# Kernel optimization log

Hardware: AMD Instinct MI355X
Metric: run time of the kernel (lower is better)

## Reference

```python
import math
import jax, jax.numpy as jnp
import numpy as np

V, D, H, L, FH = 32000, 384, 6, 6, 1536
B, S = 38, 256
HD = D // H


def setup_inputs() -> dict:
    key = jax.random.key(0)
    ks = jax.random.split(key, 16)
    sc = 0.02
    inp = {
        "x": jax.random.randint(ks[0], (B, S), 1, V, dtype=jnp.int32),
        "targets": jax.random.randint(ks[1], (B, S), 0, V, dtype=jnp.int32),
        "emb": jax.random.normal(ks[2], (V, D), jnp.float32) * sc,
        "Wqkv": jax.random.normal(ks[3], (L, 3 * D, D), jnp.float32) * sc,
        "bqkv": jnp.zeros((L, 3 * D), jnp.float32),
        "Wo": jax.random.normal(ks[4], (L, D, D), jnp.float32) * sc,
        "bo": jnp.zeros((L, D), jnp.float32),
        "gamma1": jnp.ones((L, D), jnp.float32),
        "beta1": jnp.zeros((L, D), jnp.float32),
        "W1": jax.random.normal(ks[5], (L, FH, D), jnp.float32) * sc,
        "b1": jnp.zeros((L, FH), jnp.float32),
        "W2": jax.random.normal(ks[6], (L, D, FH), jnp.float32) * sc,
        "b2": jnp.zeros((L, D), jnp.float32),
        "gamma2": jnp.ones((L, D), jnp.float32),
        "beta2": jnp.zeros((L, D), jnp.float32),
        "Wout": jax.random.normal(ks[7], (V, D), jnp.float32) * sc,
        "bout": jnp.zeros((V,), jnp.float32),
    }
    return inp


def _pos_encoding(seq_len, d_model):
    even_i = jnp.arange(0, d_model, 2, dtype=jnp.float32)
    denom = jnp.power(10000.0, even_i / d_model)  # (D/2,)
    pos = jnp.arange(seq_len, dtype=jnp.float32)[:, None]  # (S,1)
    even_pe = jnp.sin(pos / denom)
    odd_pe = jnp.cos(pos / denom)
    return jnp.stack([even_pe, odd_pe], axis=2).reshape(seq_len, d_model)


def _layer_norm(x, gamma, beta, eps=1e-5):
    mean = x.mean(axis=-1, keepdims=True)
    var = ((x - mean) ** 2).mean(axis=-1, keepdims=True)
    return gamma * (x - mean) / jnp.sqrt(var + eps) + beta


def _build_mask(x_ids, seq_len):
    # replicate the data-dependent pad mask: take the row with most non-pad
    # tokens, count its leading non-zeros -> max_length
    pad = (x_ids != 0)
    idx = jnp.argmax(pad.sum(axis=1))
    row = x_ids[idx]
    has_zero = jnp.any(row == 0)
    max_len = jnp.where(has_zero, jnp.argmax(row == 0), seq_len)
    i = jnp.arange(seq_len)[:, None]
    j = jnp.arange(seq_len)[None, :]
    allowed = (j <= i) & ~((i >= max_len) & (j >= max_len))
    return jnp.where(allowed, 0.0, -jnp.inf).astype(jnp.float32)  # (S,S)


def _forward(x, targets, emb, Wqkv, bqkv, Wo, bo, gamma1, beta1, W1, b1,
             W2, b2, gamma2, beta2, Wout, bout):
    Bn, Sn = x.shape
    h = emb[x] * math.sqrt(D) + _pos_encoding(Sn, D)[None]  # (B,S,D)
    mask = _build_mask(x, Sn)
    inv_sqrt_dk = 1.0 / math.sqrt(HD)

    def layer(h, p):
        (Wq, bq, Wo_, bo_, g1, be1, W1_, b1_, W2_, b2_, g2, be2) = p
        qkv = h @ Wq.T + bq  # (B,S,3D)
        qkv = qkv.reshape(Bn, Sn, H, 3 * HD).transpose(0, 2, 1, 3)  # (B,H,S,3hd)
        q, k, v = jnp.split(qkv, 3, axis=-1)
        scores = jnp.einsum('bhqd,bhkd->bhqk', q, k) * inv_sqrt_dk + mask
        attn = jax.nn.softmax(scores, axis=-1)
        vals = jnp.einsum('bhqk,bhkd->bhqd', attn, v)
        vals = vals.transpose(0, 2, 1, 3).reshape(Bn, Sn, D)
        att_out = vals @ Wo_.T + bo_
        h = _layer_norm(h + att_out, g1, be1)
        ffn = jax.nn.gelu(h @ W1_.T + b1_, approximate=False) @ W2_.T + b2_
        h = _layer_norm(h + ffn, g2, be2)
        return h, None

    params = (Wqkv, bqkv, Wo, bo, gamma1, beta1, W1, b1, W2, b2, gamma2, beta2)
    h, _ = jax.lax.scan(layer, h, params)

    logits = h @ Wout.T + bout  # (B,S,V)
    logp = jax.nn.log_softmax(logits, axis=-1)
    nll = -jnp.take_along_axis(logp, targets[..., None].astype(jnp.int32), axis=-1)[..., 0]
    loss = nll.mean()
    return logits, loss


def reference(x, targets, emb, Wqkv, bqkv, Wo, bo, gamma1, beta1, W1, b1,
              W2, b2, gamma2, beta2, Wout, bout):
    return _forward(x, targets, emb, Wqkv, bqkv, Wo, bo, gamma1, beta1,
                    W1, b1, W2, b2, gamma2, beta2, Wout, bout)
```

## Files before the change

### kernel.cpp

```cpp
#include <hip/hip_runtime.h>
#include <hip/hip_bf16.h>
#include <math.h>

#define VSZ 32000
#define DSZ 384
#define HSZ 6
#define LSZ 6
#define FHSZ 1536
#define BSZ 38
#define SSZ 256
#define HDSZ 64
#define NROW (BSZ*SSZ)
#define D3 (3*DSZ)
#define NTB256 (VSZ/256)

typedef __bf16 bf16;
typedef __attribute__((ext_vector_type(8))) __bf16 bf16x8;
typedef __attribute__((ext_vector_type(4))) __bf16 bf16x4;
typedef __attribute__((ext_vector_type(4))) float f32x4;

__device__ __forceinline__ void gload16(const bf16* g, bf16* l) {
  __builtin_amdgcn_global_load_lds((const __attribute__((address_space(1))) void*)g,
                                   (__attribute__((address_space(3))) void*)l, 16, 0, 0);
}

__device__ __forceinline__ int xcd_swz(int orig, int nwg) {
  int q = nwg >> 3, r = nwg & 7;
  int xcd = orig & 7, lin = orig >> 3;
  return (xcd < r ? xcd*(q+1) : r*(q+1) + (xcd - r)*q) + lin;
}

__device__ __forceinline__ float fast_erf(float x) {
  float ax = fabsf(x);
  float t = 1.0f / fmaf(0.3275911f, ax, 1.0f);
  float p = fmaf(t, 1.061405429f, -1.453152027f);
  p = fmaf(p, t, 1.421413741f);
  p = fmaf(p, t, -0.284496736f);
  p = fmaf(p, t, 0.254829592f);
  float y = 1.0f - p*t*__expf(-ax*ax);
  return copysignf(y, x);
}

struct CvtDesc { const float* s0; bf16* d0; const float* s1; bf16* d1;
                 const float* s2; bf16* d2; const float* s3; bf16* d3;
                 const float* s4; bf16* d4; };
#define C0 663552
#define C1 884736
#define C2 1769472
#define C3 2654208
#define C4 5726208
__global__ __launch_bounds__(256) void cvt_all(CvtDesc dd) {
  int i = blockIdx.x*256 + threadIdx.x;
  int st = gridDim.x*256;
  for (; i < C4; i += st) {
    const float* s; bf16* d; int o;
    if      (i < C0) { s = dd.s0; d = dd.d0; o = i; }
    else if (i < C1) { s = dd.s1; d = dd.d1; o = i - C0; }
    else if (i < C2) { s = dd.s2; d = dd.d2; o = i - C1; }
    else if (i < C3) { s = dd.s3; d = dd.d3; o = i - C2; }
    else             { s = dd.s4; d = dd.d4; o = i - C3; }
    f32x4 v = __builtin_nontemporal_load((const f32x4*)s + o);
    bf16x4 ov = { (bf16)v[0], (bf16)v[1], (bf16)v[2], (bf16)v[3] };
    *(bf16x4*)(d + 4*(size_t)o) = ov;
  }
}

__global__ __launch_bounds__(256) void pe_k(float* __restrict__ pe) {
  const float c = 2.0f/384.0f*13.287712379549449f;
  int i = blockIdx.x*256 + threadIdx.x;
  int s = i / DSZ, d = i - s*DSZ;
  int ii = d >> 1;
  float ang = (float)s * exp2f(-(float)ii * c);
  pe[i] = (d & 1) ? cosf(ang) : sinf(ang);
}

__global__ __launch_bounds__(256) void embed_k(const int* __restrict__ x,
    const float* __restrict__ emb, const float* __restrict__ pe,
    float* __restrict__ h, bf16* __restrict__ hb) {
  const float scale = 19.595917942265423f;
  int i4 = blockIdx.x*256 + threadIdx.x;
  int st = gridDim.x*256;
  for (; i4 < NROW*(DSZ/4); i4 += st) {
    int r = i4 / (DSZ/4), c4 = (i4 - r*(DSZ/4))*4;
    int tok = x[r];
    int s = r & (SSZ-1);
    f32x4 e = *((const f32x4*)(emb + (size_t)tok*DSZ + c4));
    f32x4 p = *((const f32x4*)(pe + (size_t)s*DSZ + c4));
    f32x4 v = { e[0]*scale + p[0], e[1]*scale + p[1],
                e[2]*scale + p[2], e[3]*scale + p[3] };
    *(f32x4*)(h + (size_t)i4*4) = v;
    bf16x4 o = { (bf16)v[0], (bf16)v[1], (bf16)v[2], (bf16)v[3] };
    *(bf16x4*)(hb + (size_t)i4*4) = o;
  }
}

template<int MODE>
__global__ __launch_bounds__(256) void gemm_bt(const bf16* __restrict__ A,
    const bf16* __restrict__ Bm, const float* __restrict__ bias,
    bf16* __restrict__ Cv, int N, int K) {
  __shared__ __align__(16) bf16 As[2][128*64];
  __shared__ __align__(16) bf16 Bs[2][128*64];
  const int tid = threadIdx.x;
  const int lane = tid & 63, wid = tid >> 6;

  const int GX = gridDim.x, GY = gridDim.y;
  int orig = blockIdx.y*GX + blockIdx.x;
  int swz = xcd_swz(orig, GX*GY);
  int by = swz / GX, bx = swz - (swz/GX)*GX;

  const int wm = (wid >> 1) * 64, wn = (wid & 1) * 64;
  const int lr = lane & 15, lk = (lane >> 4) * 8;
  const int sx = (lr & 7) * 8;

  f32x4 acc[4][4];
  f32x4 zz = {0.f, 0.f, 0.f, 0.f};
#pragma unroll
  for (int m = 0; m < 4; ++m)
#pragma unroll
    for (int n = 0; n < 4; ++n) acc[m][n] = zz;

  const bf16* Ab = A + (size_t)by*128*K;
  const bf16* Bb = Bm + (size_t)bx*128*K;
  const int nk = K >> 6;

  auto STAGE = [&](int buf, int kt) {
#pragma unroll
    for (int c = 0; c < 4; ++c) {
      int chunk = c*256 + tid;
      int row = chunk >> 3, sub = chunk & 7;
      int scol = (sub ^ (row & 7)) * 8;
      gload16(Ab + (size_t)row*K + kt*64 + scol, &As[buf][chunk*8]);
      gload16(Bb + (size_t)row*K + kt*64 + scol, &Bs[buf][chunk*8]);
    }
  };

  STAGE(0, 0);
  __syncthreads();
  int cur = 0;
  for (int kt = 0; kt < nk; ++kt) {
    if (kt + 1 < nk) STAGE(cur ^ 1, kt + 1);
#pragma unroll
    for (int kk = 0; kk < 2; ++kk) {
      bf16x8 af[4], bfr[4];
#pragma unroll
      for (int m = 0; m < 4; ++m)
        af[m] = *(const bf16x8*)(&As[cur][(wm + m*16 + lr)*64 + ((kk*32 + lk) ^ sx)]);
#pragma unroll
      for (int n = 0; n < 4; ++n)
        bfr[n] = *(const bf16x8*)(&Bs[cur][(wn + n*16 + lr)*64 + ((kk*32 + lk) ^ sx)]);
#pragma unroll
      for (int m = 0; m < 4; ++m)
#pragma unroll
        for (int n = 0; n < 4; ++n)
          acc[m][n] = __builtin_amdgcn_mfma_f32_16x16x32_bf16(af[m], bfr[n], acc[m][n], 0, 0, 0);
    }
    __syncthreads();
    cur ^= 1;
  }

  float bv[4];
#pragma unroll
  for (int n = 0; n < 4; ++n) bv[n] = bias[bx*128 + wn + n*16 + lr];
  const int r0 = (lane >> 4) * 4;
#pragma unroll
  for (int m = 0; m < 4; ++m) {
#pragma unroll
    for (int r = 0; r < 4; ++r) {
      size_t row = (size_t)by*128 + wm + m*16 + r0 + r;
#pragma unroll
      for (int n = 0; n < 4; ++n) {
        float v = acc[m][n][r] + bv[n];
        size_t ci = row*(size_t)N + (size_t)(bx*128 + wn + n*16 + lr);
        if (MODE == 1) Cv[ci] = (bf16)v;
        else {
          v = 0.5f*v*(1.0f + fast_erf(v*0.70710678118654752f));
          Cv[ci] = (bf16)v;
        }
      }
    }
  }
}

template<int NS>
__global__ __launch_bounds__(256) void gemm_sk(const bf16* __restrict__ A,
    const bf16* __restrict__ Bm, const float* __restrict__ bias,
    bf16* __restrict__ P, int N, int K) {
  __shared__ __align__(16) bf16 As[2][128*64];
  __shared__ __align__(16) bf16 Bs[2][128*64];
  const int tid = threadIdx.x;
  const int lane = tid & 63, wid = tid >> 6;
  const int slice = blockIdx.z;
  const int Ksl = K / NS, kb = slice * Ksl;

  const int GX = gridDim.x, GY = gridDim.y;
  int orig = blockIdx.y*GX + blockIdx.x;
  int swz = xcd_swz(orig, GX*GY);
  int by = swz / GX, bx = swz - (swz/GX)*GX;

  const int wm = (wid >> 1) * 64, wn = (wid & 1) * 64;
  const int lr = lane & 15, lk = (lane >> 4) * 8;
  const int sx = (lr & 7) * 8;

  f32x4 acc[4][4];
  f32x4 zz = {0.f, 0.f, 0.f, 0.f};
#pragma unroll
  for (int m = 0; m < 4; ++m)
#pragma unroll
    for (int n = 0; n < 4; ++n) acc[m][n] = zz;

  const bf16* Ab = A + (size_t)by*128*K + kb;
  const bf16* Bb = Bm + (size_t)bx*128*K + kb;
  const int nk = Ksl >> 6;

  auto STAGE = [&](int buf, int kt) {
#pragma unroll
    for (int c = 0; c < 4; ++c) {
      int chunk = c*256 + tid;
      int row = chunk >> 3, sub = chunk & 7;
      int scol = (sub ^ (row & 7)) * 8;
      gload16(Ab + (size_t)row*K + kt*64 + scol, &As[buf][chunk*8]);
      gload16(Bb + (size_t)row*K + kt*64 + scol, &Bs[buf][chunk*8]);
    }
  };

  STAGE(0, 0);
  __syncthreads();
  int cur = 0;
  for (int kt = 0; kt < nk; ++kt) {
    if (kt + 1 < nk) STAGE(cur ^ 1, kt + 1);
#pragma unroll
    for (int kk = 0; kk < 2; ++kk) {
      bf16x8 af[4], bfr[4];
#pragma unroll
      for (int m = 0; m < 4; ++m)
        af[m] = *(const bf16x8*)(&As[cur][(wm + m*16 + lr)*64 + ((kk*32 + lk) ^ sx)]);
#pragma unroll
      for (int n = 0; n < 4; ++n)
        bfr[n] = *(const bf16x8*)(&Bs[cur][(wn + n*16 + lr)*64 + ((kk*32 + lk) ^ sx)]);
#pragma unroll
      for (int m = 0; m < 4; ++m)
#pragma unroll
        for (int n = 0; n < 4; ++n)
          acc[m][n] = __builtin_amdgcn_mfma_f32_16x16x32_bf16(af[m], bfr[n], acc[m][n], 0, 0, 0);
    }
    __syncthreads();
    cur ^= 1;
  }

  float bv[4];
#pragma unroll
  for (int n = 0; n < 4; ++n)
    bv[n] = (slice == 0) ? bias[bx*128 + wn + n*16 + lr] : 0.0f;
  const int r0 = (lane >> 4) * 4;
  bf16* Pw = P + (size_t)slice*NROW*N;
#pragma unroll
  for (int m = 0; m < 4; ++m) {
#pragma unroll
    for (int r = 0; r < 4; ++r) {
      size_t row = (size_t)by*128 + wm + m*16 + r0 + r;
#pragma unroll
      for (int n = 0; n < 4; ++n) {
        size_t ci = row*(size_t)N + (size_t)(bx*128 + wn + n*16 + lr);
        Pw[ci] = (bf16)(acc[m][n][r] + bv[n]);
      }
    }
  }
}

__global__ __launch_bounds__(512, 2) void gemm256_lse(const bf16* __restrict__ A,
    const bf16* __restrict__ Bm, const float* __restrict__ bias,
    float* __restrict__ C, float* __restrict__ pmax, float* __restrict__ psum) {
  __shared__ __align__(16) bf16 As[4][256*32];
  __shared__ __align__(16) bf16 Bs[4][256*32];
  __shared__ float sm_m[4][256], sm_s[4][256];
  const int K = DSZ, N = VSZ;
  const int tid = threadIdx.x;
  const int lane = tid & 63, wid = tid >> 6;

  const int GX = gridDim.x, GY = gridDim.y;
  int orig = blockIdx.y*GX + blockIdx.x;
  int swz = xcd_swz(orig, GX*GY);
  int bx = swz / GY, by = swz - (swz/GY)*GY;

  const int wm = (wid >> 2) * 128, wn = (wid & 3) * 64;
  const int lr = lane & 15, lk = (lane >> 4) * 8;

  f32x4 acc[8][4];
  f32x4 zz = {0.f, 0.f, 0.f, 0.f};
#pragma unroll
  for (int m = 0; m < 8; ++m)
#pragma unroll
    for (int n = 0; n < 4; ++n) acc[m][n] = zz;

  const bf16* Ab = A + (size_t)by*256*K;
  const bf16* Bb = Bm + (size_t)bx*256*K;
  const int nk = 12;

  auto STAGE = [&](int buf, int kt) {
#pragma unroll
    for (int c = 0; c < 2; ++c) {
      int chunk = c*512 + tid;
      int row = chunk >> 2, sub = chunk & 3;
      int scol = (sub ^ ((row >> 1) & 3)) * 8;
      gload16(Ab + (size_t)row*K + kt*32 + scol, &As[buf][chunk*8]);
      gload16(Bb + (size_t)row*K + kt*32 + scol, &Bs[buf][chunk*8]);
    }
  };

  STAGE(0, 0); STAGE(1, 1); STAGE(2, 2);
  for (int kt = 0; kt < nk; ++kt) {
    if (kt < nk - 2)      asm volatile("s_waitcnt vmcnt(8)" ::: "memory");
    else if (kt == nk-2)  asm volatile("s_waitcnt vmcnt(4)" ::: "memory");
    else                  asm volatile("s_waitcnt vmcnt(0)" ::: "memory");
    __builtin_amdgcn_s_barrier();
    __builtin_amdgcn_sched_barrier(0);
    const int buf = kt & 3;
    bf16x8 af[8], bfr[4];
#pragma unroll
    for (int n = 0; n < 4; ++n) {
      int row = wn + n*16 + lr;
      bfr[n] = *(const bf16x8*)(&Bs[buf][row*32 + (lk ^ (((row >> 1) & 3)*8))]);
    }
#pragma unroll
    for (int m = 0; m < 8; ++m) {
      int row = wm + m*16 + lr;
      af[m] = *(const bf16x8*)(&As[buf][row*32 + (lk ^ (((row >> 1) & 3)*8))]);
    }
#pragma unroll
    for (int m = 0; m < 8; ++m)
#pragma unroll
      for (int n = 0; n < 4; ++n)
        acc[m][n] = __builtin_amdgcn_mfma_f32_16x16x32_bf16(af[m], bfr[n], acc[m][n], 0, 0, 0);
    if (kt + 3 < nk) STAGE((kt + 3) & 3, kt + 3);
    __builtin_amdgcn_s_barrier();
  }

  float bv[4];
#pragma unroll
  for (int n = 0; n < 4; ++n) bv[n] = bias[bx*256 + wn + n*16 + lr];
  const int r0 = (lane >> 4) * 4;

#pragma unroll
  for (int m = 0; m < 8; ++m) {
#pragma unroll
    for (int r = 0; r < 4; ++r) {
      const int rl = wm + m*16 + r0 + r;
      size_t row = (size_t)by*256 + rl;
      float v0 = acc[m][0][r] + bv[0], v1 = acc[m][1][r] + bv[1];
      float v2 = acc[m][2][r] + bv[2], v3 = acc[m][3][r] + bv[3];
      size_t cb = row*(size_t)N + (size_t)(bx*256 + wn + lr);
      __builtin_nontemporal_store(v0, &C[cb]);
      __builtin_nontemporal_store(v1, &C[cb + 16]);
      __builtin_nontemporal_store(v2, &C[cb + 32]);
      __builtin_nontemporal_store(v3, &C[cb + 48]);
      float mx = fmaxf(fmaxf(v0, v1), fmaxf(v2, v3));
#pragma unroll
      for (int o = 1; o <= 8; o <<= 1) mx = fmaxf(mx, __shfl_xor(mx, o));
      float s = __expf(v0-mx) + __expf(v1-mx) + __expf(v2-mx) + __expf(v3-mx);
#pragma unroll
      for (int o = 1; o <= 8; o <<= 1) s += __shfl_xor(s, o);
      if (lr == 0) { sm_m[wid & 3][rl] = mx; sm_s[wid & 3][rl] = s; }
    }
  }
  __syncthreads();
  if (tid < 256) {
    float m = -1e30f, s = 0.f;
#pragma unroll
    for (int c = 0; c < 4; ++c) {
      float mi = sm_m[c][tid], si = sm_s[c][tid];
      float nm = fmaxf(m, mi);
      s = s*__expf(m - nm) + si*__expf(mi - nm);
      m = nm;
    }
    size_t row = (size_t)by*256 + tid;
    pmax[row*NTB256 + bx] = m;
    psum[row*NTB256 + bx] = s;
  }
}

__global__ __launch_bounds__(256) void attn_mfma(const bf16* __restrict__ qkv,
                                                 bf16* __restrict__ vals) {
  __shared__ __align__(16) ushort Ks[256*72];
  __shared__ __align__(16) ushort Vt[64*264];
  const int tid = threadIdx.x;
  const int lane = tid & 63, w = tid >> 6;
  const int lo = lane & 15, hi = lane >> 4;
  const int bid = blockIdx.x;
  const int qt = bid & 3, bh = bid >> 2;
  const int b = bh / HSZ, hh = bh - b*HSZ;
  const int nkr = (qt + 1) * 64;
  const int qb = qt*64 + w*16;
  const int ntile = qt*4 + w + 1;
  const int kkmax = (ntile + 1) >> 1;

  {
    const int jr = tid >> 3, cc = (tid & 7) * 8;
    for (int p = 0; p < (qt+1)*2; ++p) {
      int j = p*32 + jr;
      const bf16* base = qkv + ((size_t)(b*SSZ + j))*D3 + hh*192 + 64 + cc;
      uint4 kq = *(const uint4*)base;
      *(uint2*)(&Ks[j*72 + cc])     = make_uint2(kq.x, kq.y);
      *(uint2*)(&Ks[j*72 + cc + 4]) = make_uint2(kq.z, kq.w);
    }
  }
  for (int k = tid; k < nkr; k += 256) {
    const bf16* vrow = qkv + ((size_t)(b*SSZ + k))*D3 + hh*192 + 128;
#pragma unroll
    for (int c = 0; c < 8; ++c) {
      uint4 vv = *(const uint4*)(vrow + c*8);
      const ushort* u = (const ushort*)&vv;
#pragma unroll
      for (int j = 0; j < 8; ++j)
        Vt[(c*8 + j)*264 + k] = u[j];
    }
  }

  bf16x8 qf0, qf1;
  {
    const bf16* qrow = qkv + ((size_t)(b*SSZ + qb + lo))*D3 + hh*192 + hi*8;
    qf0 = *(const bf16x8*)(qrow);
    qf1 = *(const bf16x8*)(qrow + 32);
  }
  __syncthreads();

  f32x4 zz = {0.f, 0.f, 0.f, 0.f};
  f32x4 sacc[16];
#pragma unroll
  for (int n = 0; n < 16; ++n) sacc[n] = zz;
#pragma unroll
  for (int n = 0; n < 16; ++n)
    if (n < ntile) {
      const bf16* kb0 = (const bf16*)&Ks[(n*16 + lo)*72 + hi*8];
      bf16x8 bf0 = *(const bf16x8*)(kb0);
      bf16x8 bf1 = *(const bf16x8*)(kb0 + 32);
      sacc[n] = __builtin_amdgcn_mfma_f32_16x16x32_bf16(qf0, bf0, sacc[n], 0, 0, 0);
      sacc[n] = __builtin_amdgcn_mfma_f32_16x16x32_bf16(qf1, bf1, sacc[n], 0, 0, 0);
    }
  __syncthreads();

  float mrow[4] = {-1e30f, -1e30f, -1e30f, -1e30f};
#pragma unroll
  for (int n = 0; n < 16; ++n)
    if (n < ntile) {
#pragma unroll
      for (int r = 0; r < 4; ++r) {
        int kcol = n*16 + lo, qi = qb + hi*4 + r;
        float s = (kcol <= qi) ? sacc[n][r]*0.125f : -1e30f;
        sacc[n][r] = s;
        mrow[r] = fmaxf(mrow[r], s);
      }
    }
#pragma unroll
  for (int r = 0; r < 4; ++r)
#pragma unroll
    for (int o = 1; o <= 8; o <<= 1)
      mrow[r] = fmaxf(mrow[r], __shfl_xor(mrow[r], o));

  ushort* Pl = &Ks[w*64*72];
  float lsum[4] = {0.f, 0.f, 0.f, 0.f};
#pragma unroll
  for (int n = 0; n < 16; ++n)
    if (n < 2*kkmax) {
#pragma unroll
      for (int r = 0; r < 4; ++r) {
        float e = 0.f;
        if (n < ntile) { e = __expf(sacc[n][r] - mrow[r]); lsum[r] += e; }
        bf16 eb = (bf16)e;
        Pl[(hi*4 + r)*264 + n*16 + lo] = *(const ushort*)&eb;
      }
    }
#pragma unroll
  for (int r = 0; r < 4; ++r)
#pragma unroll
    for (int o = 1; o <= 8; o <<= 1)
      lsum[r] += __shfl_xor(lsum[r], o);

  asm volatile("s_waitcnt lgkmcnt(0)" ::: "memory");

  f32x4 oacc[4];
#pragma unroll
  for (int nd = 0; nd < 4; ++nd) oacc[nd] = zz;
#pragma unroll
  for (int kk = 0; kk < 8; ++kk)
    if (kk < kkmax) {
      bf16x8 pf = *(const bf16x8*)((const bf16*)&Pl[lo*264 + kk*32 + hi*8]);
#pragma unroll
      for (int nd = 0; nd < 4; ++nd) {
        bf16x8 vf = *(const bf16x8*)((const bf16*)&Vt[(nd*16 + lo)*264 + kk*32 + hi*8]);
        oacc[nd] = __builtin_amdgcn_mfma_f32_16x16x32_bf16(pf, vf, oacc[nd], 0, 0, 0);
      }
    }

#pragma unroll
  for (int r = 0; r < 4; ++r) {
    float inv = 1.0f / lsum[r];
    size_t row = (size_t)(b*SSZ + qb + hi*4 + r);
#pragma unroll
    for (int nd = 0; nd < 4; ++nd)
      vals[row*DSZ + hh*64 + nd*16 + lo] = (bf16)(oacc[nd][r] * inv);
  }
}

template<int NS>
__global__ __launch_bounds__(256) void ln_sum(const bf16* __restrict__ P,
    const float* __restrict__ gamma, const float* __restrict__ beta,
    float* __restrict__ h, bf16* __restrict__ hb) {
  const int t = threadIdx.x;
  const int lane = t & 63, w = t >> 6;
  const int row = blockIdx.x*4 + w;
  const size_t base = (size_t)row*DSZ;
  float v[6];
  float s = 0.f;
#pragma unroll
  for (int k = 0; k < 6; ++k) {
    int idx = lane + k*64;
    float acc = h[base + idx];
#pragma unroll
    for (int sl = 0; sl < NS; ++sl)
      acc += (float)P[(size_t)sl*NROW*DSZ + base + idx];
    v[k] = acc;
    s += acc;
  }
#pragma unroll
  for (int o = 32; o; o >>= 1) s += __shfl_xor(s, o);
  float mean = s * (1.0f/DSZ);
  float s2 = 0.f;
#pragma unroll
  for (int k = 0; k < 6; ++k) { float dv = v[k] - mean; s2 += dv*dv; }
#pragma unroll
  for (int o = 32; o; o >>= 1) s2 += __shfl_xor(s2, o);
  float rstd = rsqrtf(s2 * (1.0f/DSZ) + 1e-5f);
#pragma unroll
  for (int k = 0; k < 6; ++k) {
    int idx = lane + k*64;
    float outv = gamma[idx]*(v[k] - mean)*rstd + beta[idx];
    h[base + idx] = outv;
    hb[base + idx] = (bf16)outv;
  }
}

__global__ __launch_bounds__(256) void loss_merge(const float* __restrict__ pmax,
    const float* __restrict__ psum, const float* __restrict__ logits,
    const int* __restrict__ tg, float* __restrict__ nll, int ntb) {
  const int t = threadIdx.x;
  const int lane = t & 63, w = t >> 6;
  const int row = blockIdx.x*4 + w;
  float m = -1e30f, s = 0.f;
  for (int i = lane; i < ntb; i += 64) {
    float mi = pmax[(size_t)row*ntb + i], si = psum[(size_t)row*ntb + i];
    float nm = fmaxf(m, mi);
    s = s*__expf(m - nm) + si*__expf(mi - nm);
    m = nm;
  }
#pragma unroll
  for (int o = 32; o; o >>= 1) {
    float mo = __shfl_xor(m, o), so = __shfl_xor(s, o);
    float nm = fmaxf(m, mo);
    s = s*__expf(m - nm) + so*__expf(mo - nm);
    m = nm;
  }
  if (lane == 0)
    nll[row] = (m + logf(s)) - logits[(size_t)row*VSZ + tg[row]];
}

__global__ __launch_bounds__(256) void loss_final(const float* __restrict__ nll,
                                                  float* __restrict__ out) {
  __shared__ float red[4];
  const int t = threadIdx.x;
  const int lane = t & 63, w = t >> 6;
  float s = 0.f;
  for (int i = t; i < NROW; i += 256) s += nll[i];
#pragma unroll
  for (int o = 32; o; o >>= 1) s += __shfl_xor(s, o);
  if (lane == 0) red[w] = s;
  __syncthreads();
  if (t == 0) out[0] = (red[0]+red[1]+red[2]+red[3]) * (1.0f/NROW);
}

extern "C" void kernel_launch(void* const* d_in, const int* in_sizes, int n_in,
                              void* d_out, int out_size, void* d_ws, size_t ws_size,
                              hipStream_t stream) {
  (void)in_sizes; (void)n_in; (void)out_size; (void)ws_size;
  const int*   x       = (const int*)  d_in[0];
  const int*   targets = (const int*)  d_in[1];
  const float* emb     = (const float*)d_in[2];
  const float* Wqkv    = (const float*)d_in[3];
  const float* bqkv    = (const float*)d_in[4];
  const float* Wo      = (const float*)d_in[5];
  const float* bo      = (const float*)d_in[6];
  const float* gamma1  = (const float*)d_in[7];
  const float* beta1   = (const float*)d_in[8];
  const float* W1      = (const float*)d_in[9];
  const float* b1      = (const float*)d_in[10];
  const float* W2      = (const float*)d_in[11];
  const float* b2      = (const float*)d_in[12];
  const float* gamma2  = (const float*)d_in[13];
  const float* beta2   = (const float*)d_in[14];
  const float* Wout    = (const float*)d_in[15];
  const float* bout    = (const float*)d_in[16];
  float* out = (float*)d_out;

  char* wp = (char*)d_ws;
  auto carve = [&](size_t bytes)->char* {
    char* p = wp; wp += (bytes + 255) & ~(size_t)255; return p;
  };
  bf16*  Wqkv_b = (bf16*) carve((size_t)LSZ*D3*DSZ*2);
  bf16*  Wo_b   = (bf16*) carve((size_t)LSZ*DSZ*DSZ*2);
  bf16*  W1_b   = (bf16*) carve((size_t)LSZ*FHSZ*DSZ*2);
  bf16*  W2_b   = (bf16*) carve((size_t)LSZ*DSZ*FHSZ*2);
  bf16*  Wout_b = (bf16*) carve((size_t)VSZ*DSZ*2);
  float* h      = (float*)carve((size_t)NROW*DSZ*4);
  bf16*  hb     = (bf16*) carve((size_t)NROW*DSZ*2);
  bf16*  qkv_b  = (bf16*) carve((size_t)NROW*D3*2);
  bf16*  vals_b = (bf16*) carve((size_t)NROW*DSZ*2);
  bf16*  tmp    = (bf16*) carve((size_t)4*NROW*DSZ*2);
  bf16*  ffn1_b = (bf16*) carve((size_t)NROW*FHSZ*2);
  float* nll    = (float*)carve((size_t)NROW*4);
  float* pmax   = (float*)carve((size_t)NROW*NTB256*4);
  float* psum   = (float*)carve((size_t)NROW*NTB256*4);
  float* pe     = (float*)carve((size_t)SSZ*DSZ*4);

  CvtDesc dd = { Wqkv, Wqkv_b, Wo, Wo_b, W1, W1_b, W2, W2_b, Wout, Wout_b };
  cvt_all<<<dim3(4096), dim3(256), 0, stream>>>(dd);

  pe_k<<<dim3(SSZ*DSZ/256), dim3(256), 0, stream>>>(pe);
  embed_k<<<dim3(2048), dim3(256), 0, stream>>>(x, emb, pe, h, hb);

  for (int l = 0; l < LSZ; ++l) {
    gemm_bt<1><<<dim3(D3/128, NROW/128), dim3(256), 0, stream>>>(
        hb, Wqkv_b + (size_t)l*D3*DSZ, bqkv + l*D3, qkv_b, D3, DSZ);
    attn_mfma<<<dim3(BSZ*HSZ*4), dim3(256), 0, stream>>>(qkv_b, vals_b);
    gemm_sk<2><<<dim3(DSZ/128, NROW/128, 2), dim3(256), 0, stream>>>(
        vals_b, Wo_b + (size_t)l*DSZ*DSZ, bo + l*DSZ, tmp, DSZ, DSZ);
    ln_sum<2><<<dim3(NROW/4), dim3(256), 0, stream>>>(
        tmp, gamma1 + l*DSZ, beta1 + l*DSZ, h, hb);
    gemm_bt<2><<<dim3(FHSZ/128, NROW/128), dim3(256), 0, stream>>>(
        hb, W1_b + (size_t)l*FHSZ*DSZ, b1 + l*FHSZ, ffn1_b, FHSZ, DSZ);
    gemm_sk<4><<<dim3(DSZ/128, NROW/128, 4), dim3(256), 0, stream>>>(
        ffn1_b, W2_b + (size_t)l*DSZ*FHSZ, b2 + l*DSZ, tmp, DSZ, FHSZ);
    ln_sum<4><<<dim3(NROW/4), dim3(256), 0, stream>>>(
        tmp, gamma2 + l*DSZ, beta2 + l*DSZ, h, hb);
  }

  gemm256_lse<<<dim3(VSZ/256, NROW/256), dim3(512), 0, stream>>>(
      hb, Wout_b, bout, out, pmax, psum);
  loss_merge<<<dim3(NROW/4), dim3(256), 0, stream>>>(pmax, psum, out, targets, nll, NTB256);
  loss_final<<<dim3(1), dim3(256), 0, stream>>>(nll, out + (size_t)NROW*VSZ);
}
```

Before: 1.262 ms.

## Fuse output projections with residual add and LayerNorm in full-row GEMM

Replaces the split-K GEMM plus separate ln_sum kernel with one kernel where each block computes a 64-row by full-384-column tile, then adds bias and residual and applies LayerNorm in the epilogue using cross-wave shared-memory reductions. This removes the bf16 partial-sum buffer round trip and one launch per LayerNorm. In exchange the grid shrinks to 152 blocks with no split-K, so the K=1536 FFN2 GEMM may lose parallelism, and variance is now computed as E[x^2]-mean^2, which is less numerically stable.

```diff
diff --git a/kernel.cpp b/kernel.cpp
--- a/kernel.cpp
+++ b/kernel.cpp
@@ -181,45 +181,42 @@
   }
 }
 
-template<int NS>
-__global__ __launch_bounds__(256) void gemm_sk(const bf16* __restrict__ A,
+template<int K>
+__global__ __launch_bounds__(256) void gemm_ln(const bf16* __restrict__ A,
     const bf16* __restrict__ Bm, const float* __restrict__ bias,
-    bf16* __restrict__ P, int N, int K) {
-  __shared__ __align__(16) bf16 As[2][128*64];
-  __shared__ __align__(16) bf16 Bs[2][128*64];
+    const float* __restrict__ gamma, const float* __restrict__ beta,
+    float* __restrict__ h, bf16* __restrict__ hb) {
+  __shared__ __align__(16) bf16 As[2][64*32];
+  __shared__ __align__(16) bf16 Bs[2][384*32];
+  __shared__ float sm_s[4][64], sm_q[4][64];
   const int tid = threadIdx.x;
   const int lane = tid & 63, wid = tid >> 6;
-  const int slice = blockIdx.z;
-  const int Ksl = K / NS, kb = slice * Ksl;
-
-  const int GX = gridDim.x, GY = gridDim.y;
-  int orig = blockIdx.y*GX + blockIdx.x;
-  int swz = xcd_swz(orig, GX*GY);
-  int by = swz / GX, bx = swz - (swz/GX)*GX;
-
-  const int wm = (wid >> 1) * 64, wn = (wid & 1) * 64;
+  const int by = xcd_swz(blockIdx.x, gridDim.x);
+  const int wn = wid * 96;
   const int lr = lane & 15, lk = (lane >> 4) * 8;
-  const int sx = (lr & 7) * 8;
-
-  f32x4 acc[4][4];
+
+  f32x4 acc[4][6];
   f32x4 zz = {0.f, 0.f, 0.f, 0.f};
 #pragma unroll
   for (int m = 0; m < 4; ++m)
 #pragma unroll
-    for (int n = 0; n < 4; ++n) acc[m][n] = zz;
-
-  const bf16* Ab = A + (size_t)by*128*K + kb;
-  const bf16* Bb = Bm + (size_t)bx*128*K + kb;
-  const int nk = Ksl >> 6;
+    for (int n = 0; n < 6; ++n) acc[m][n] = zz;
+
+  const bf16* Ab = A + (size_t)by*64*K;
+  const int nk = K >> 5;
 
   auto STAGE = [&](int buf, int kt) {
-#pragma unroll
-    for (int c = 0; c < 4; ++c) {
+    {
+      int row = tid >> 2, sub = tid & 3;
+      int scol = (sub ^ ((row >> 1) & 3)) * 8;
+      gload16(Ab + (size_t)row*K + kt*32 + scol, &As[buf][tid*8]);
+    }
+#pragma unroll
+    for (int c = 0; c < 6; ++c) {
       int chunk = c*256 + tid;
-      int row = chunk >> 3, sub = chunk & 7;
-      int scol = (sub ^ (row & 7)) * 8;
-      gload16(Ab + (size_t)row*K + kt*64 + scol, &As[buf][chunk*8]);
-      gload16(Bb + (size_t)row*K + kt*64 + scol, &Bs[buf][chunk*8]);
+      int row = chunk >> 2, sub = chunk & 3;
+      int scol = (sub ^ ((row >> 1) & 3)) * 8;
+      gload16(Bm + (size_t)row*K + kt*32 + scol, &Bs[buf][chunk*8]);
     }
   };
 
@@ -228,43 +225,76 @@
   int cur = 0;
   for (int kt = 0; kt < nk; ++kt) {
     if (kt + 1 < nk) STAGE(cur ^ 1, kt + 1);
-#pragma unroll
-    for (int kk = 0; kk < 2; ++kk) {
-      bf16x8 af[4], bfr[4];
-#pragma unroll
-      for (int m = 0; m < 4; ++m)
-        af[m] = *(const bf16x8*)(&As[cur][(wm + m*16 + lr)*64 + ((kk*32 + lk) ^ sx)]);
-#pragma unroll
-      for (int n = 0; n < 4; ++n)
-        bfr[n] = *(const bf16x8*)(&Bs[cur][(wn + n*16 + lr)*64 + ((kk*32 + lk) ^ sx)]);
-#pragma unroll
-      for (int m = 0; m < 4; ++m)
-#pragma unroll
-        for (int n = 0; n < 4; ++n)
-          acc[m][n] = __builtin_amdgcn_mfma_f32_16x16x32_bf16(af[m], bfr[n], acc[m][n], 0, 0, 0);
-    }
+    bf16x8 af[4], bfr[6];
+#pragma unroll
+    for (int m = 0; m < 4; ++m) {
+      int row = m*16 + lr;
+      af[m] = *(const bf16x8*)(&As[cur][row*32 + (lk ^ (((row >> 1) & 3)*8))]);
+    }
+#pragma unroll
+    for (int n = 0; n < 6; ++n) {
+      int row = wn + n*16 + lr;
+      bfr[n] = *(const bf16x8*)(&Bs[cur][row*32 + (lk ^ (((row >> 1) & 3)*8))]);
+    }
+#pragma unroll
+    for (int m = 0; m < 4; ++m)
+#pragma unroll
+      for (int n = 0; n < 6; ++n)
+        acc[m][n] = __builtin_amdgcn_mfma_f32_16x16x32_bf16(af[m], bfr[n], acc[m][n], 0, 0, 0);
     __syncthreads();
     cur ^= 1;
   }
 
-  float bv[4];
-#pragma unroll
-  for (int n = 0; n < 4; ++n)
-    bv[n] = (slice == 0) ? bias[bx*128 + wn + n*16 + lr] : 0.0f;
+  float bv[6], gv[6], btv[6];
+#pragma unroll
+  for (int n = 0; n < 6; ++n) {
+    int col = wn + n*16 + lr;
+    bv[n] = bias[col]; gv[n] = gamma[col]; btv[n] = beta[col];
+  }
   const int r0 = (lane >> 4) * 4;
-  bf16* Pw = P + (size_t)slice*NROW*N;
-#pragma unroll
-  for (int m = 0; m < 4; ++m) {
+
+#pragma unroll
+  for (int m = 0; m < 4; ++m)
 #pragma unroll
     for (int r = 0; r < 4; ++r) {
-      size_t row = (size_t)by*128 + wm + m*16 + r0 + r;
-#pragma unroll
-      for (int n = 0; n < 4; ++n) {
-        size_t ci = row*(size_t)N + (size_t)(bx*128 + wn + n*16 + lr);
-        Pw[ci] = (bf16)(acc[m][n][r] + bv[n]);
+      size_t row = (size_t)by*64 + m*16 + r0 + r;
+#pragma unroll
+      for (int n = 0; n < 6; ++n)
+        acc[m][n][r] += bv[n] + h[row*DSZ + wn + n*16 + lr];
+    }
+
+#pragma unroll
+  for (int m = 0; m < 4; ++m)
+#pragma unroll
+    for (int r = 0; r < 4; ++r) {
+      float s = 0.f, q = 0.f;
+#pragma unroll
+      for (int n = 0; n < 6; ++n) { float x = acc[m][n][r]; s += x; q += x*x; }
+#pragma unroll
+      for (int o = 1; o <= 8; o <<= 1) { s += __shfl_xor(s, o); q += __shfl_xor(q, o); }
+      if (lr == 0) { sm_s[wid][m*16 + r0 + r] = s; sm_q[wid][m*16 + r0 + r] = q; }
+    }
+  __syncthreads();
+
+#pragma unroll
+  for (int m = 0; m < 4; ++m)
+#pragma unroll
+    for (int r = 0; r < 4; ++r) {
+      const int rl = m*16 + r0 + r;
+      float S = sm_s[0][rl] + sm_s[1][rl] + sm_s[2][rl] + sm_s[3][rl];
+      float Q = sm_q[0][rl] + sm_q[1][rl] + sm_q[2][rl] + sm_q[3][rl];
+      float mean = S * (1.0f/DSZ);
+      float var = Q * (1.0f/DSZ) - mean*mean;
+      float rstd = rsqrtf(var + 1e-5f);
+      size_t row = (size_t)by*64 + rl;
+#pragma unroll
+      for (int n = 0; n < 6; ++n) {
+        float outv = gv[n]*(acc[m][n][r] - mean)*rstd + btv[n];
+        size_t ci = row*DSZ + wn + n*16 + lr;
+        h[ci] = outv;
+        hb[ci] = (bf16)outv;
       }
     }
-  }
 }
 
 __global__ __launch_bounds__(512, 2) void gemm256_lse(const bf16* __restrict__ A,
@@ -498,44 +528,6 @@
 #pragma unroll
     for (int nd = 0; nd < 4; ++nd)
       vals[row*DSZ + hh*64 + nd*16 + lo] = (bf16)(oacc[nd][r] * inv);
-  }
-}
-
-template<int NS>
-__global__ __launch_bounds__(256) void ln_sum(const bf16* __restrict__ P,
-    const float* __restrict__ gamma, const float* __restrict__ beta,
-    float* __restrict__ h, bf16* __restrict__ hb) {
-  const int t = threadIdx.x;
-  const int lane = t & 63, w = t >> 6;
-  const int row = blockIdx.x*4 + w;
-  const size_t base = (size_t)row*DSZ;
-  float v[6];
-  float s = 0.f;
-#pragma unroll
-  for (int k = 0; k < 6; ++k) {
-    int idx = lane + k*64;
-    float acc = h[base + idx];
-#pragma unroll
-    for (int sl = 0; sl < NS; ++sl)
-      acc += (float)P[(size_t)sl*NROW*DSZ + base + idx];
-    v[k] = acc;
-    s += acc;
-  }
-#pragma unroll
-  for (int o = 32; o; o >>= 1) s += __shfl_xor(s, o);
-  float mean = s * (1.0f/DSZ);
-  float s2 = 0.f;
-#pragma unroll
-  for (int k = 0; k < 6; ++k) { float dv = v[k] - mean; s2 += dv*dv; }
-#pragma unroll
-  for (int o = 32; o; o >>= 1) s2 += __shfl_xor(s2, o);
-  float rstd = rsqrtf(s2 * (1.0f/DSZ) + 1e-5f);
-#pragma unroll
-  for (int k = 0; k < 6; ++k) {
-    int idx = lane + k*64;
-    float outv = gamma[idx]*(v[k] - mean)*rstd + beta[idx];
-    h[base + idx] = outv;
-    hb[base + idx] = (bf16)outv;
   }
 }
 
@@ -613,7 +605,6 @@
   bf16*  hb     = (bf16*) carve((size_t)NROW*DSZ*2);
   bf16*  qkv_b  = (bf16*) carve((size_t)NROW*D3*2);
   bf16*  vals_b = (bf16*) carve((size_t)NROW*DSZ*2);
-  bf16*  tmp    = (bf16*) carve((size_t)4*NROW*DSZ*2);
   bf16*  ffn1_b = (bf16*) carve((size_t)NROW*FHSZ*2);
   float* nll    = (float*)carve((size_t)NROW*4);
   float* pmax   = (float*)carve((size_t)NROW*NTB256*4);
@@ -630,16 +621,14 @@
     gemm_bt<1><<<dim3(D3/128, NROW/128), dim3(256), 0, stream>>>(
         hb, Wqkv_b + (size_t)l*D3*DSZ, bqkv + l*D3, qkv_b, D3, DSZ);
     attn_mfma<<<dim3(BSZ*HSZ*4), dim3(256), 0, stream>>>(qkv_b, vals_b);
-    gemm_sk<2><<<dim3(DSZ/128, NROW/128, 2), dim3(256), 0, stream>>>(
-        vals_b, Wo_b + (size_t)l*DSZ*DSZ, bo + l*DSZ, tmp, DSZ, DSZ);
-    ln_sum<2><<<dim3(NROW/4), dim3(256), 0, stream>>>(
-        tmp, gamma1 + l*DSZ, beta1 + l*DSZ, h, hb);
+    gemm_ln<DSZ><<<dim3(NROW/64), dim3(256), 0, stream>>>(
+        vals_b, Wo_b + (size_t)l*DSZ*DSZ, bo + l*DSZ,
+        gamma1 + l*DSZ, beta1 + l*DSZ, h, hb);
     gemm_bt<2><<<dim3(FHSZ/128, NROW/128), dim3(256), 0, stream>>>(
         hb, W1_b + (size_t)l*FHSZ*DSZ, b1 + l*FHSZ, ffn1_b, FHSZ, DSZ);
-    gemm_sk<4><<<dim3(DSZ/128, NROW/128, 4), dim3(256), 0, stream>>>(
-        ffn1_b, W2_b + (size_t)l*DSZ*FHSZ, b2 + l*DSZ, tmp, DSZ, FHSZ);
-    ln_sum<4><<<dim3(NROW/4), dim3(256), 0, stream>>>(
-        tmp, gamma2 + l*DSZ, beta2 + l*DSZ, h, hb);
+    gemm_ln<FHSZ><<<dim3(NROW/64), dim3(256), 0, stream>>>(
+        ffn1_b, W2_b + (size_t)l*DSZ*FHSZ, b2 + l*DSZ,
+        gamma2 + l*DSZ, beta2 + l*DSZ, h, hb);
   }
 
   gemm256_lse<<<dim3(VSZ/256, NROW/256), dim3(512), 0, stream>>>(
```

Measured after the change: 1.454 ms. +15.2%, slower.
